# Kernel optimization log

Measured on AMD Instinct MI355X. Metric: run time of the kernel, lower is better.

The kernel has to match this reference:

```python
import jax, jax.numpy as jnp
import numpy as np

EPS_REG = 0.05      # epsilon (entropic regularization), learn_epsilon=False
NUM_ITERS = 20      # Sinkhorn iterations
MESH_ITERS = 3      # MESH sharpening iterations


def setup_inputs() -> dict:
    key = jax.random.key(0)
    k1, k2, k3, k4 = jax.random.split(key, 4)
    B, K, M, D = 2048, 64, 64, 256
    slots_q = jax.random.normal(k1, (B, K, D), dtype=jnp.float32)
    slots_r = jax.random.normal(k2, (B, M, D), dtype=jnp.float32)
    mask_q = jnp.ones((B, K), dtype=jnp.float32)
    mask_r = jnp.ones((B, M), dtype=jnp.float32)
    W1 = jax.random.normal(k3, (D, D), dtype=jnp.float32) * (1.0 / np.sqrt(D))
    b1 = jnp.zeros((D,), dtype=jnp.float32)
    W2 = jax.random.normal(k4, (D, D), dtype=jnp.float32) * (1.0 / np.sqrt(D))
    b2 = jnp.zeros((D,), dtype=jnp.float32)
    return {"slots_q": slots_q, "slots_r": slots_r, "mask_q": mask_q,
            "mask_r": mask_r, "W1": W1, "b1": b1, "W2": W2, "b2": b2}


def _cost_proj(x, W1, b1, W2, b2):
    h = jax.nn.relu(jnp.einsum('bnd,de->bne', x, W1) + b1)
    return jnp.einsum('bnd,de->bne', h, W2) + b2


def _cdist(q, r):
    # Euclidean pairwise distance: [B,K,M]
    q2 = jnp.sum(q * q, axis=-1)                      # [B,K]
    r2 = jnp.sum(r * r, axis=-1)                      # [B,M]
    qr = jnp.einsum('bkd,bmd->bkm', q, r)             # [B,K,M]
    d2 = q2[:, :, None] + r2[:, None, :] - 2.0 * qr
    return jnp.sqrt(jnp.clip(d2, 0.0))


def _sinkhorn(C, mask_q, mask_r):
    log_K = -C / EPS_REG
    log_K = log_K + jnp.log(jnp.clip(mask_q, 1e-8))[:, :, None]
    log_K = log_K + jnp.log(jnp.clip(mask_r, 1e-8))[:, None, :]
    B, K, M = C.shape
    la0 = jnp.zeros((B, K, 1), dtype=C.dtype)
    lb0 = jnp.zeros((B, 1, M), dtype=C.dtype)

    def body(i, carry):
        la, lb = carry
        la = -jax.nn.logsumexp(log_K + lb, axis=2, keepdims=True)
        lb = -jax.nn.logsumexp(log_K + la, axis=1, keepdims=True)
        return (la, lb)

    la, lb = jax.lax.fori_loop(0, NUM_ITERS, body, (la0, lb0))
    return jnp.exp(log_K + la + lb)


def _mesh(T):
    def body(i, T):
        Ts = T * T
        Ts = Ts / (jnp.sum(Ts, axis=-1, keepdims=True) + 1e-8)
        Ts = Ts / (jnp.sum(Ts, axis=-2, keepdims=True) + 1e-8)
        return Ts
    return jax.lax.fori_loop(0, MESH_ITERS, body, T)


def reference(slots_q, slots_r, mask_q, mask_r, W1, b1, W2, b2):
    q_proj = _cost_proj(slots_q, W1, b1, W2, b2)
    r_proj = _cost_proj(slots_r, W1, b1, W2, b2)
    C = _cdist(q_proj, r_proj)                        # [B,K,M]
    T = _sinkhorn(C, mask_q, mask_r)                  # [B,K,M]
    T_hard = _mesh(T)
    transport_cost = jnp.sum(T_hard * C, axis=(-1, -2))   # [B]
    similarity = jax.nn.sigmoid(-transport_cost)           # [B]
    return similarity, T_hard, C, transport_cost
```

## Files before the change

kernel.cpp:

```cpp
#include <hip/hip_runtime.h>


typedef __attribute__((ext_vector_type(8))) short s16x8;
typedef __attribute__((ext_vector_type(4))) float f32x4;

#define OFF_T  2048
#define OFF_C  (2048 + 2048 * 4096)
#define OFF_TC (2048 + 2 * 2048 * 4096)

__device__ __forceinline__ unsigned short f2bf(float x) {
  unsigned u = __builtin_bit_cast(unsigned, x);
  u += 0x7fffu + ((u >> 16) & 1u);
  return (unsigned short)(u >> 16);
}
__device__ __forceinline__ unsigned cvtpk(float lo, float hi) {
  unsigned r;
  asm("v_cvt_pk_bf16_f32 %0, %1, %2" : "=v"(r) : "v"(lo), "v"(hi));
  return r;
}

#define MFMA16(a, b, c) __builtin_amdgcn_mfma_f32_16x16x32_bf16((a), (b), (c), 0, 0, 0)

__global__ void __launch_bounds__(256)
prep_w_kernel(const float* __restrict__ W1, const float* __restrict__ W2,
              short* __restrict__ W1p, short* __restrict__ W2p) {
  int i = blockIdx.x * 256 + threadIdx.x;
  int k = i >> 8, col = i & 255;
  int p = (col >> 4) * 4096 + (k >> 5) * 512 +
          (((k >> 3) & 3) * 16 + (col & 15)) * 8 + (k & 7);
  W1p[p] = (short)f2bf(W1[i]);
  W2p[p] = (short)f2bf(W2[i]);
}

template <int RF>
__device__ __forceinline__ void gemm_kloop(const short* __restrict__ wb,
                                           const char* sm, int abase0, int asw,
                                           int koff0, f32x4 (&acc)[4][RF]) {
  s16x8 bw[4][4];
#pragma unroll
  for (int p = 0; p < 4; ++p)
#pragma unroll
    for (int nf = 0; nf < 4; ++nf)
      bw[p][nf] = *(const s16x8*)(wb + nf * 4096 + p * 512);
#pragma unroll
  for (int ks = 0; ks < 8; ++ks) {
    const int ko = (ks * 64 + koff0) ^ asw;
    s16x8 af[RF];
#pragma unroll
    for (int rf = 0; rf < RF; ++rf)
      af[rf] = *(const s16x8*)(sm + rf * 8192 + abase0 + ko);
#pragma unroll
    for (int rf = 0; rf < RF; ++rf)
#pragma unroll
      for (int nf = 0; nf < 4; ++nf)
        acc[nf][rf] = MFMA16(bw[ks & 3][nf], af[rf], acc[nf][rf]);
    if (ks < 4) {
#pragma unroll
      for (int nf = 0; nf < 4; ++nf)
        bw[ks & 3][nf] = *(const s16x8*)(wb + nf * 4096 + (ks + 4) * 512);
    }
  }
}

__global__ void __launch_bounds__(256, 2)
proj_cost_kernel(const float* __restrict__ slots_q, const float* __restrict__ slots_r,
                 const short* __restrict__ W1p, const short* __restrict__ W2p,
                 const float* __restrict__ b1, const float* __restrict__ b2,
                 float* __restrict__ out) {
  __shared__ char smem[65536];
  float* nbuf = (float*)smem;

  const int b    = blockIdx.x;
  const int tid  = threadIdx.x;
  const int wv   = tid >> 6;
  const int lane = tid & 63;
  const int l15  = lane & 15;
  const int lhi  = lane >> 4;

  {
    const float* sq = slots_q + (size_t)b * 16384;
    const float* sr = slots_r + (size_t)b * 16384;
#pragma unroll
    for (int half = 0; half < 2; ++half) {
      float4 tmp[16];
#pragma unroll
      for (int i = 0; i < 16; ++i) {
        int idx4 = tid + 256 * (half * 16 + i);
        tmp[i] = (half == 0) ? *(const float4*)(sq + idx4 * 4)
                             : *(const float4*)(sr + (idx4 - 4096) * 4);
      }
#pragma unroll
      for (int i = 0; i < 16; ++i) {
        int idx4 = tid + 256 * (half * 16 + i);
        int row = idx4 >> 6;
        int colb = (idx4 & 63) * 8;
        *(uint2*)(smem + row * 512 + (colb ^ ((row & 7) << 4))) =
            make_uint2(cvtpk(tmp[i].x, tmp[i].y), cvtpk(tmp[i].z, tmp[i].w));
      }
    }
  }
  __syncthreads();

  const int abase0 = l15 * 512;
  const int asw    = (l15 & 7) << 4;
  const int koff0  = lhi * 16;
  const short* wb1 = W1p + wv * 4 * 4096 + lane * 8;
  const short* wb2 = W2p + wv * 4 * 4096 + lane * 8;

  float4 b1v[4], b2v[4];
#pragma unroll
  for (int ef = 0; ef < 4; ++ef) {
    b1v[ef] = *(const float4*)(b1 + wv * 64 + ef * 16 + lhi * 4);
    b2v[ef] = *(const float4*)(b2 + wv * 64 + ef * 16 + lhi * 4);
  }

  const f32x4 z4 = {0.f, 0.f, 0.f, 0.f};
  f32x4 acc[4][8];

#pragma unroll
  for (int ef = 0; ef < 4; ++ef)
#pragma unroll
    for (int rf = 0; rf < 8; ++rf) acc[ef][rf] = z4;
  gemm_kloop<8>(wb1, smem, abase0, asw, koff0, acc);
  __syncthreads();
#pragma unroll
  for (int ef = 0; ef < 4; ++ef) {
    const int eb = (wv * 64 + ef * 16 + lhi * 4) * 2;
#pragma unroll
    for (int rf = 0; rf < 8; ++rf) {
      float a0 = fmaxf(acc[ef][rf][0] + b1v[ef].x, 0.0f);
      float a1 = fmaxf(acc[ef][rf][1] + b1v[ef].y, 0.0f);
      float a2 = fmaxf(acc[ef][rf][2] + b1v[ef].z, 0.0f);
      float a3 = fmaxf(acc[ef][rf][3] + b1v[ef].w, 0.0f);
      *(uint2*)(smem + rf * 8192 + abase0 + (eb ^ asw)) =
          make_uint2(cvtpk(a0, a1), cvtpk(a2, a3));
    }
  }
  __syncthreads();

#pragma unroll
  for (int ef = 0; ef < 4; ++ef)
#pragma unroll
    for (int rf = 0; rf < 8; ++rf) acc[ef][rf] = z4;
  gemm_kloop<8>(wb2, smem, abase0, asw, koff0, acc);
  __syncthreads();

  float pn[8] = {0.f, 0.f, 0.f, 0.f, 0.f, 0.f, 0.f, 0.f};
#pragma unroll
  for (int ef = 0; ef < 4; ++ef) {
    const int eb = (wv * 64 + ef * 16 + lhi * 4) * 2;
#pragma unroll
    for (int rf = 0; rf < 8; ++rf) {
      float a0 = acc[ef][rf][0] + b2v[ef].x;
      float a1 = acc[ef][rf][1] + b2v[ef].y;
      float a2 = acc[ef][rf][2] + b2v[ef].z;
      float a3 = acc[ef][rf][3] + b2v[ef].w;
      pn[rf] += a0 * a0 + a1 * a1 + a2 * a2 + a3 * a3;
      *(uint2*)(smem + rf * 8192 + abase0 + (eb ^ asw)) =
          make_uint2(cvtpk(a0, a1), cvtpk(a2, a3));
    }
  }
#pragma unroll
  for (int rf = 0; rf < 8; ++rf) {
    pn[rf] += __shfl_xor(pn[rf], 16);
    pn[rf] += __shfl_xor(pn[rf], 32);
  }
  __syncthreads();

  f32x4 accC[4];
#pragma unroll
  for (int n = 0; n < 4; ++n) accC[n] = z4;
#pragma unroll
  for (int ks = 0; ks < 8; ++ks) {
    const int ko = (ks * 64 + koff0) ^ asw;
    s16x8 aQ = *(const s16x8*)(smem + wv * 8192 + abase0 + ko);
#pragma unroll
    for (int n = 0; n < 4; ++n) {
      s16x8 bR = *(const s16x8*)(smem + 32768 + n * 8192 + abase0 + ko);
      accC[n] = MFMA16(aQ, bR, accC[n]);
    }
  }
  __syncthreads();

  if (lhi == 0) {
#pragma unroll
    for (int rf = 0; rf < 8; ++rf) nbuf[wv * 128 + rf * 16 + l15] = pn[rf];
  }
  __syncthreads();

  f32x4 nq = z4;
#pragma unroll
  for (int w = 0; w < 4; ++w)
    nq += *(const f32x4*)(nbuf + w * 128 + wv * 16 + lhi * 4);
  float nR[4];
#pragma unroll
  for (int n = 0; n < 4; ++n) {
    float s = 0.0f;
#pragma unroll
    for (int w = 0; w < 4; ++w) s += nbuf[w * 128 + 64 + n * 16 + l15];
    nR[n] = s;
  }

  float* Cb = out + OFF_C + (size_t)b * 4096;
#pragma unroll
  for (int n = 0; n < 4; ++n)
#pragma unroll
    for (int j = 0; j < 4; ++j) {
      float d2 = nq[j] + nR[n] - 2.0f * accC[n][j];
      Cb[(wv * 16 + lhi * 4 + j) * 64 + n * 16 + l15] = sqrtf(fmaxf(d2, 0.0f));
    }
}

__global__ void __launch_bounds__(256, 4)
sinkhorn_solve(const float* __restrict__ mask_r, float* __restrict__ out) {
  __shared__ float tile[64 * 65];
  __shared__ float u_arr[64], w_arr[64], red[4];

  const int b    = blockIdx.x;
  const int tid  = threadIdx.x;
  const int wv   = tid >> 6;
  const int lane = tid & 63;
  const int rk   = tid >> 2;
  const int g    = tid & 3;
  const int e0   = g * 16;

  const float* Cb = out + OFF_C + (size_t)b * 4096;

#pragma unroll
  for (int i = 0; i < 16; ++i) {
    int idx = tid + 256 * i;
    tile[(idx >> 6) * 65 + (idx & 63)] = Cb[idx];
  }
  if (tid < 64) w_arr[tid] = __logf(fmaxf(mask_r[(size_t)b * 64 + tid], 1e-8f));
  __syncthreads();

  float cn[16], cc[16];
#pragma unroll
  for (int i = 0; i < 16; ++i) {
    cn[i] = tile[rk * 65 + e0 + i] * -20.0f;
    cc[i] = tile[(e0 + i) * 65 + rk] * -20.0f;
  }

  for (int it = 0; it < 20; ++it) {
    {
      float v[16];
#pragma unroll
      for (int i = 0; i < 16; ++i) v[i] = cn[i] + w_arr[e0 + i];
      float mx = v[0];
#pragma unroll
      for (int i = 1; i < 16; ++i) mx = fmaxf(mx, v[i]);
      float s = 0.0f;
#pragma unroll
      for (int i = 0; i < 16; ++i) s += __expf(v[i] - mx);
#pragma unroll
      for (int d = 1; d < 4; d <<= 1) {
        float mo = __shfl_xor(mx, d), so = __shfl_xor(s, d);
        float nm = fmaxf(mx, mo);
        s = s * __expf(mx - nm) + so * __expf(mo - nm);
        mx = nm;
      }
      if (g == 0) u_arr[rk] = -(mx + __logf(s));
    }
    __syncthreads();
    {
      float v[16];
#pragma unroll
      for (int i = 0; i < 16; ++i) v[i] = cc[i] + u_arr[e0 + i];
      float mx = v[0];
#pragma unroll
      for (int i = 1; i < 16; ++i) mx = fmaxf(mx, v[i]);
      float s = 0.0f;
#pragma unroll
      for (int i = 0; i < 16; ++i) s += __expf(v[i] - mx);
#pragma unroll
      for (int d = 1; d < 4; d <<= 1) {
        float mo = __shfl_xor(mx, d), so = __shfl_xor(s, d);
        float nm = fmaxf(mx, mo);
        s = s * __expf(mx - nm) + so * __expf(mo - nm);
        mx = nm;
      }
      if (g == 0) w_arr[rk] = -(mx + __logf(s));
    }
    __syncthreads();
  }

  float t[16];
  {
    float uk = u_arr[rk];
#pragma unroll
    for (int i = 0; i < 16; ++i) t[i] = __expf(cn[i] + uk + w_arr[e0 + i]);
  }
  for (int it = 0; it < 3; ++it) {
    if (it > 0) {
      __syncthreads();
#pragma unroll
      for (int i = 0; i < 16; ++i) t[i] = tile[rk * 65 + e0 + i];
    }
    float s = 0.0f;
#pragma unroll
    for (int i = 0; i < 16; ++i) { t[i] *= t[i]; s += t[i]; }
    s += __shfl_xor(s, 1); s += __shfl_xor(s, 2);
    float inv = 1.0f / (s + 1e-8f);
#pragma unroll
    for (int i = 0; i < 16; ++i) tile[rk * 65 + e0 + i] = t[i] * inv;
    __syncthreads();
    float tc[16]; float cs = 0.0f;
#pragma unroll
    for (int i = 0; i < 16; ++i) { tc[i] = tile[(e0 + i) * 65 + rk]; cs += tc[i]; }
    cs += __shfl_xor(cs, 1); cs += __shfl_xor(cs, 2);
    inv = 1.0f / (cs + 1e-8f);
#pragma unroll
    for (int i = 0; i < 16; ++i) tile[(e0 + i) * 65 + rk] = tc[i] * inv;
  }
  __syncthreads();

  {
    float part = 0.0f;
#pragma unroll
    for (int i = 0; i < 16; ++i)
      part += tile[rk * 65 + e0 + i] * (cn[i] * -0.05f);
#pragma unroll
    for (int d = 1; d < 64; d <<= 1) part += __shfl_xor(part, d);
    if (lane == 0) red[wv] = part;
  }
  __syncthreads();
  if (tid == 0) {
    float tc = red[0] + red[1] + red[2] + red[3];
    out[OFF_TC + b] = tc;
    out[b] = 1.0f / (1.0f + __expf(tc));
  }
  {
    float* Tout = out + OFF_T + (size_t)b * 4096;
#pragma unroll
    for (int i = 0; i < 16; ++i) {
      int idx = tid + 256 * i;
      Tout[idx] = tile[(idx >> 6) * 65 + (idx & 63)];
    }
  }
}

extern "C" void kernel_launch(void* const* d_in, const int* in_sizes, int n_in,
                              void* d_out, int out_size, void* d_ws, size_t ws_size,
                              hipStream_t stream) {
  const float* slots_q = (const float*)d_in[0];
  const float* slots_r = (const float*)d_in[1];
  const float* mask_r = (const float*)d_in[3];
  const float* W1 = (const float*)d_in[4];
  const float* b1 = (const float*)d_in[5];
  const float* W2 = (const float*)d_in[6];
  const float* b2 = (const float*)d_in[7];

  short* W1p = (short*)d_ws;
  short* W2p = W1p + 65536;

  prep_w_kernel<<<256, 256, 0, stream>>>(W1, W2, W1p, W2p);
  proj_cost_kernel<<<2048, 256, 0, stream>>>(slots_q, slots_r, W1p, W2p, b1, b2,
                                             (float*)d_out);
  sinkhorn_solve<<<2048, 256, 0, stream>>>(mask_r, (float*)d_out);
}
```

Before: 244.6 us.

## Make projection kernel persistent over 4 batches with register prefetch of next inputs

```diff
diff --git a/kernel.cpp b/kernel.cpp
--- a/kernel.cpp
+++ b/kernel.cpp
@@ -32,10 +32,9 @@
   W2p[p] = (short)f2bf(W2[i]);
 }
 
-template <int RF>
 __device__ __forceinline__ void gemm_kloop(const short* __restrict__ wb,
                                            const char* sm, int abase0, int asw,
-                                           int koff0, f32x4 (&acc)[4][RF]) {
+                                           int koff0, f32x4 (&acc)[4][8]) {
   s16x8 bw[4][4];
 #pragma unroll
   for (int p = 0; p < 4; ++p)
@@ -45,12 +44,12 @@
 #pragma unroll
   for (int ks = 0; ks < 8; ++ks) {
     const int ko = (ks * 64 + koff0) ^ asw;
-    s16x8 af[RF];
-#pragma unroll
-    for (int rf = 0; rf < RF; ++rf)
+    s16x8 af[8];
+#pragma unroll
+    for (int rf = 0; rf < 8; ++rf)
       af[rf] = *(const s16x8*)(sm + rf * 8192 + abase0 + ko);
 #pragma unroll
-    for (int rf = 0; rf < RF; ++rf)
+    for (int rf = 0; rf < 8; ++rf)
 #pragma unroll
       for (int nf = 0; nf < 4; ++nf)
         acc[nf][rf] = MFMA16(bw[ks & 3][nf], af[rf], acc[nf][rf]);
@@ -70,37 +69,12 @@
   __shared__ char smem[65536];
   float* nbuf = (float*)smem;
 
-  const int b    = blockIdx.x;
   const int tid  = threadIdx.x;
   const int wv   = tid >> 6;
   const int lane = tid & 63;
   const int l15  = lane & 15;
   const int lhi  = lane >> 4;
 
-  {
-    const float* sq = slots_q + (size_t)b * 16384;
-    const float* sr = slots_r + (size_t)b * 16384;
-#pragma unroll
-    for (int half = 0; half < 2; ++half) {
-      float4 tmp[16];
-#pragma unroll
-      for (int i = 0; i < 16; ++i) {
-        int idx4 = tid + 256 * (half * 16 + i);
-        tmp[i] = (half == 0) ? *(const float4*)(sq + idx4 * 4)
-                             : *(const float4*)(sr + (idx4 - 4096) * 4);
-      }
-#pragma unroll
-      for (int i = 0; i < 16; ++i) {
-        int idx4 = tid + 256 * (half * 16 + i);
-        int row = idx4 >> 6;
-        int colb = (idx4 & 63) * 8;
-        *(uint2*)(smem + row * 512 + (colb ^ ((row & 7) << 4))) =
-            make_uint2(cvtpk(tmp[i].x, tmp[i].y), cvtpk(tmp[i].z, tmp[i].w));
-      }
-    }
-  }
-  __syncthreads();
-
   const int abase0 = l15 * 512;
   const int asw    = (l15 & 7) << 4;
   const int koff0  = lhi * 16;
@@ -115,100 +89,143 @@
   }
 
   const f32x4 z4 = {0.f, 0.f, 0.f, 0.f};
-  f32x4 acc[4][8];
-
-#pragma unroll
-  for (int ef = 0; ef < 4; ++ef)
-#pragma unroll
-    for (int rf = 0; rf < 8; ++rf) acc[ef][rf] = z4;
-  gemm_kloop<8>(wb1, smem, abase0, asw, koff0, acc);
-  __syncthreads();
-#pragma unroll
-  for (int ef = 0; ef < 4; ++ef) {
-    const int eb = (wv * 64 + ef * 16 + lhi * 4) * 2;
+
+  float4 xq[16], xr[16];
+  {
+    const float* sq = slots_q + (size_t)blockIdx.x * 16384;
+    const float* sr = slots_r + (size_t)blockIdx.x * 16384;
+#pragma unroll
+    for (int i = 0; i < 16; ++i) {
+      int idx4 = tid + 256 * i;
+      xq[i] = *(const float4*)(sq + idx4 * 4);
+      xr[i] = *(const float4*)(sr + idx4 * 4);
+    }
+  }
+
+#pragma unroll 1
+  for (int t = 0; t < 4; ++t) {
+    const int b = blockIdx.x + t * 512;
+
+#pragma unroll
+    for (int i = 0; i < 16; ++i) {
+      int idx4 = tid + 256 * i;
+      int row = idx4 >> 6;
+      int colb = (idx4 & 63) * 8;
+      int sw = (row & 7) << 4;
+      *(uint2*)(smem + row * 512 + (colb ^ sw)) =
+          make_uint2(cvtpk(xq[i].x, xq[i].y), cvtpk(xq[i].z, xq[i].w));
+      *(uint2*)(smem + (row + 64) * 512 + (colb ^ sw)) =
+          make_uint2(cvtpk(xr[i].x, xr[i].y), cvtpk(xr[i].z, xr[i].w));
+    }
+    __syncthreads();
+
+    f32x4 acc[4][8];
+
+#pragma unroll
+    for (int ef = 0; ef < 4; ++ef)
+#pragma unroll
+      for (int rf = 0; rf < 8; ++rf) acc[ef][rf] = z4;
+    gemm_kloop(wb1, smem, abase0, asw, koff0, acc);
+    __syncthreads();
+#pragma unroll
+    for (int ef = 0; ef < 4; ++ef) {
+      const int eb = (wv * 64 + ef * 16 + lhi * 4) * 2;
+#pragma unroll
+      for (int rf = 0; rf < 8; ++rf) {
+        float a0 = fmaxf(acc[ef][rf][0] + b1v[ef].x, 0.0f);
+        float a1 = fmaxf(acc[ef][rf][1] + b1v[ef].y, 0.0f);
+        float a2 = fmaxf(acc[ef][rf][2] + b1v[ef].z, 0.0f);
+        float a3 = fmaxf(acc[ef][rf][3] + b1v[ef].w, 0.0f);
+        *(uint2*)(smem + rf * 8192 + abase0 + (eb ^ asw)) =
+            make_uint2(cvtpk(a0, a1), cvtpk(a2, a3));
+      }
+    }
+    __syncthreads();
+
+#pragma unroll
+    for (int ef = 0; ef < 4; ++ef)
+#pragma unroll
+      for (int rf = 0; rf < 8; ++rf) acc[ef][rf] = z4;
+    gemm_kloop(wb2, smem, abase0, asw, koff0, acc);
+    __syncthreads();
+
+    float pn[8] = {0.f, 0.f, 0.f, 0.f, 0.f, 0.f, 0.f, 0.f};
+#pragma unroll
+    for (int ef = 0; ef < 4; ++ef) {
+      const int eb = (wv * 64 + ef * 16 + lhi * 4) * 2;
+#pragma unroll
+      for (int rf = 0; rf < 8; ++rf) {
+        float a0 = acc[ef][rf][0] + b2v[ef].x;
+        float a1 = acc[ef][rf][1] + b2v[ef].y;
+        float a2 = acc[ef][rf][2] + b2v[ef].z;
+        float a3 = acc[ef][rf][3] + b2v[ef].w;
+        pn[rf] += a0 * a0 + a1 * a1 + a2 * a2 + a3 * a3;
+        *(uint2*)(smem + rf * 8192 + abase0 + (eb ^ asw)) =
+            make_uint2(cvtpk(a0, a1), cvtpk(a2, a3));
+      }
+    }
 #pragma unroll
     for (int rf = 0; rf < 8; ++rf) {
-      float a0 = fmaxf(acc[ef][rf][0] + b1v[ef].x, 0.0f);
-      float a1 = fmaxf(acc[ef][rf][1] + b1v[ef].y, 0.0f);
-      float a2 = fmaxf(acc[ef][rf][2] + b1v[ef].z, 0.0f);
-      float a3 = fmaxf(acc[ef][rf][3] + b1v[ef].w, 0.0f);
-      *(uint2*)(smem + rf * 8192 + abase0 + (eb ^ asw)) =
-          make_uint2(cvtpk(a0, a1), cvtpk(a2, a3));
-    }
-  }
-  __syncthreads();
-
-#pragma unroll
-  for (int ef = 0; ef < 4; ++ef)
-#pragma unroll
-    for (int rf = 0; rf < 8; ++rf) acc[ef][rf] = z4;
-  gemm_kloop<8>(wb2, smem, abase0, asw, koff0, acc);
-  __syncthreads();
-
-  float pn[8] = {0.f, 0.f, 0.f, 0.f, 0.f, 0.f, 0.f, 0.f};
-#pragma unroll
-  for (int ef = 0; ef < 4; ++ef) {
-    const int eb = (wv * 64 + ef * 16 + lhi * 4) * 2;
-#pragma unroll
-    for (int rf = 0; rf < 8; ++rf) {
-      float a0 = acc[ef][rf][0] + b2v[ef].x;
-      float a1 = acc[ef][rf][1] + b2v[ef].y;
-      float a2 = acc[ef][rf][2] + b2v[ef].z;
-      float a3 = acc[ef][rf][3] + b2v[ef].w;
-      pn[rf] += a0 * a0 + a1 * a1 + a2 * a2 + a3 * a3;
-      *(uint2*)(smem + rf * 8192 + abase0 + (eb ^ asw)) =
-          make_uint2(cvtpk(a0, a1), cvtpk(a2, a3));
-    }
-  }
-#pragma unroll
-  for (int rf = 0; rf < 8; ++rf) {
-    pn[rf] += __shfl_xor(pn[rf], 16);
-    pn[rf] += __shfl_xor(pn[rf], 32);
-  }
-  __syncthreads();
-
-  f32x4 accC[4];
-#pragma unroll
-  for (int n = 0; n < 4; ++n) accC[n] = z4;
-#pragma unroll
-  for (int ks = 0; ks < 8; ++ks) {
-    const int ko = (ks * 64 + koff0) ^ asw;
-    s16x8 aQ = *(const s16x8*)(smem + wv * 8192 + abase0 + ko);
+      pn[rf] += __shfl_xor(pn[rf], 16);
+      pn[rf] += __shfl_xor(pn[rf], 32);
+    }
+    __syncthreads();
+
+    if (t < 3) {
+      const float* sqn = slots_q + (size_t)(b + 512) * 16384;
+      const float* srn = slots_r + (size_t)(b + 512) * 16384;
+#pragma unroll
+      for (int i = 0; i < 16; ++i) {
+        int idx4 = tid + 256 * i;
+        xq[i] = *(const float4*)(sqn + idx4 * 4);
+        xr[i] = *(const float4*)(srn + idx4 * 4);
+      }
+    }
+
+    f32x4 accC[4];
+#pragma unroll
+    for (int n = 0; n < 4; ++n) accC[n] = z4;
+#pragma unroll
+    for (int ks = 0; ks < 8; ++ks) {
+      const int ko = (ks * 64 + koff0) ^ asw;
+      s16x8 aQ = *(const s16x8*)(smem + wv * 8192 + abase0 + ko);
+#pragma unroll
+      for (int n = 0; n < 4; ++n) {
+        s16x8 bR = *(const s16x8*)(smem + 32768 + n * 8192 + abase0 + ko);
+        accC[n] = MFMA16(aQ, bR, accC[n]);
+      }
+    }
+    __syncthreads();
+
+    if (lhi == 0) {
+#pragma unroll
+      for (int rf = 0; rf < 8; ++rf) nbuf[wv * 128 + rf * 16 + l15] = pn[rf];
+    }
+    __syncthreads();
+
+    f32x4 nq = z4;
+#pragma unroll
+    for (int w = 0; w < 4; ++w)
+      nq += *(const f32x4*)(nbuf + w * 128 + wv * 16 + lhi * 4);
+    float nR[4];
 #pragma unroll
     for (int n = 0; n < 4; ++n) {
-      s16x8 bR = *(const s16x8*)(smem + 32768 + n * 8192 + abase0 + ko);
-      accC[n] = MFMA16(aQ, bR, accC[n]);
-    }
-  }
-  __syncthreads();
-
-  if (lhi == 0) {
-#pragma unroll
-    for (int rf = 0; rf < 8; ++rf) nbuf[wv * 128 + rf * 16 + l15] = pn[rf];
-  }
-  __syncthreads();
-
-  f32x4 nq = z4;
-#pragma unroll
-  for (int w = 0; w < 4; ++w)
-    nq += *(const f32x4*)(nbuf + w * 128 + wv * 16 + lhi * 4);
-  float nR[4];
-#pragma unroll
-  for (int n = 0; n < 4; ++n) {
-    float s = 0.0f;
-#pragma unroll
-    for (int w = 0; w < 4; ++w) s += nbuf[w * 128 + 64 + n * 16 + l15];
-    nR[n] = s;
-  }
-
-  float* Cb = out + OFF_C + (size_t)b * 4096;
-#pragma unroll
-  for (int n = 0; n < 4; ++n)
-#pragma unroll
-    for (int j = 0; j < 4; ++j) {
-      float d2 = nq[j] + nR[n] - 2.0f * accC[n][j];
-      Cb[(wv * 16 + lhi * 4 + j) * 64 + n * 16 + l15] = sqrtf(fmaxf(d2, 0.0f));
-    }
+      float s = 0.0f;
+#pragma unroll
+      for (int w = 0; w < 4; ++w) s += nbuf[w * 128 + 64 + n * 16 + l15];
+      nR[n] = s;
+    }
+
+    float* Cb = out + OFF_C + (size_t)b * 4096;
+#pragma unroll
+    for (int n = 0; n < 4; ++n)
+#pragma unroll
+      for (int j = 0; j < 4; ++j) {
+        float d2 = nq[j] + nR[n] - 2.0f * accC[n][j];
+        Cb[(wv * 16 + lhi * 4 + j) * 64 + n * 16 + l15] = sqrtf(fmaxf(d2, 0.0f));
+      }
+    __syncthreads();
+  }
 }
 
 __global__ void __launch_bounds__(256, 4)
@@ -354,7 +371,7 @@
   short* W2p = W1p + 65536;
 
   prep_w_kernel<<<256, 256, 0, stream>>>(W1, W2, W1p, W2p);
-  proj_cost_kernel<<<2048, 256, 0, stream>>>(slots_q, slots_r, W1p, W2p, b1, b2,
-                                             (float*)d_out);
+  proj_cost_kernel<<<512, 256, 0, stream>>>(slots_q, slots_r, W1p, W2p, b1, b2,
+                                            (float*)d_out);
   sinkhorn_solve<<<2048, 256, 0, stream>>>(mask_r, (float*)d_out);
 }
```

Result: slower. 388.5 us (+58.8%).
